# Performance work log

Measured on AMD Instinct MI355X. Metric: run time of the kernel, lower is better.

## Reference

```python
import jax, jax.numpy as jnp
import numpy as np

N_HEADS = 16
NEG = -1e9  # matches torch masked_fill value


def setup_inputs() -> dict:
    key = jax.random.key(0)
    ks = jax.random.split(key, 8)
    B, S, E = 4, 1024, 1024
    x = jax.random.normal(ks[0], (B, S, E), dtype=jnp.float32)
    event_lengths = jax.random.randint(ks[1], (B,), 1, S + 1)
    scale = 1.0 / np.sqrt(E)
    Wq = jax.random.normal(ks[2], (E, E), dtype=jnp.float32) * scale
    bq = jnp.zeros((E,), dtype=jnp.float32)
    Wk = jax.random.normal(ks[3], (E, E), dtype=jnp.float32) * scale
    bk = jnp.zeros((E,), dtype=jnp.float32)
    Wv = jax.random.normal(ks[4], (E, E), dtype=jnp.float32) * scale
    bv = jnp.zeros((E,), dtype=jnp.float32)
    return {"x": x, "Wq": Wq, "bq": bq, "Wk": Wk, "bk": bk,
            "Wv": Wv, "bv": bv, "event_lengths": event_lengths}


def reference(x, Wq, bq, Wk, bk, Wv, bv, event_lengths):
    B, S, E = x.shape
    H = N_HEADS
    D = E // H
    # fused projections, then split heads: [B,S,E] -> [B,H,S,D]
    def split(t):
        return t.reshape(B, S, H, D).transpose(0, 2, 1, 3)
    q = split(x @ Wq + bq)
    k = split(x @ Wk + bk)
    v = split(x @ Wv + bv)
    scores = jnp.einsum('bhsd,bhtd->bhst', q, k) / jnp.sqrt(jnp.float32(D))
    # rectangular length mask: valid iff row < len AND col < len
    idx = jnp.arange(S)
    valid = idx[None, :] < event_lengths[:, None]           # [B,S]
    mask = valid[:, :, None] & valid[:, None, :]            # [B,S,S]
    scores = jnp.where(mask[:, None, :, :], scores, NEG)
    attn = jax.nn.softmax(scores, axis=-1)
    out = jnp.einsum('bhst,bhtd->bhsd', attn, v)            # [B,H,S,D]
    # concat heads (== torch.cat over head outputs); NOTE: summarize proj is
    # dead code in the original (its result is overwritten), dropout is eval-identity
    return out.transpose(0, 2, 1, 3).reshape(B, S, E)
```

## Files before the change

kernel.cpp:

```cpp
#include <hip/hip_runtime.h>
#include <stdint.h>


using u16     = unsigned short;
using half8   = __attribute__((ext_vector_type(8))) _Float16;
using floatx4 = __attribute__((ext_vector_type(4))) float;

#define MFMA16(a, b, c) __builtin_amdgcn_mfma_f32_16x16x32_f16(a, b, c, 0, 0, 0)

__device__ __forceinline__ u16 f2h(float f) {
  _Float16 h = (_Float16)f; u16 u; __builtin_memcpy(&u, &h, 2); return u;
}

__device__ __forceinline__ void async_cp16(void* lds, const void* g) {
  __builtin_amdgcn_global_load_lds(
      (__attribute__((address_space(1))) uint32_t*)(uintptr_t)g,
      (__attribute__((address_space(3))) uint32_t*)(uint32_t)(uintptr_t)lds,
      16, 0, 0);
}

__global__ void k_prep(const float* __restrict__ x, u16* __restrict__ xh,
                       const float* __restrict__ w0, const float* __restrict__ w1,
                       const float* __restrict__ w2,
                       u16* __restrict__ o0, u16* __restrict__ o1,
                       u16* __restrict__ o2, float* __restrict__ vsum) {
  __shared__ float t[32][33];
  const int bx = blockIdx.x;
  if (bx < 4096) {
    int i = (bx * 256 + threadIdx.x) * 4;
    float4 v = *(const float4*)(x + i);
    ushort4 hv;
    hv.x = f2h(v.x);
    hv.y = f2h(v.y);
    hv.z = f2h(v.z);
    hv.w = f2h(v.w);
    *(ushort4*)(xh + i) = hv;
    if (bx == 0) {
      float4 z = {0.f, 0.f, 0.f, 0.f};
#pragma unroll
      for (int e = 0; e < 4; e++) ((float4*)vsum)[threadIdx.x * 4 + e] = z;
    }
    return;
  }
  const int id = bx - 4096;
  const int z = id >> 10, rem = id & 1023;
  const float* W = z == 0 ? w0 : (z == 1 ? w1 : w2);
  u16* oh = z == 0 ? o0 : (z == 1 ? o1 : o2);
  const int kb = (rem & 31) * 32, nb = (rem >> 5) * 32;
  const int tx = threadIdx.x & 31, ty = threadIdx.x >> 5;
  for (int r = ty; r < 32; r += 8) t[r][tx] = W[(kb + r) * 1024 + nb + tx];
  __syncthreads();
  for (int r = ty; r < 32; r += 8)
    oh[(nb + r) * 1024 + kb + tx] = f2h(t[tx][r]);
}

__launch_bounds__(256, 4)
__global__ void k_proj(const u16* __restrict__ xh,
                       const u16* __restrict__ wqT, const u16* __restrict__ wkT,
                       const u16* __restrict__ wvT,
                       const float* __restrict__ bq, const float* __restrict__ bk,
                       const float* __restrict__ bv,
                       const int* __restrict__ elen,
                       u16* __restrict__ qh, u16* __restrict__ kh,
                       u16* __restrict__ vth, float* __restrict__ vsum) {
  __shared__ u16 Sm[17408];
  const int z = blockIdx.z;
  const int m0 = blockIdx.x * 128, n0 = blockIdx.y * 128;
  if (z != 2 && (m0 & 1023) >= elen[m0 >> 10]) return;

  const u16* wT = z == 0 ? wqT : (z == 1 ? wkT : wvT);
  const float* bias = z == 0 ? bq : (z == 1 ? bk : bv);
  u16* oh = z == 0 ? qh : (z == 1 ? kh : vth);
  const float oscale = (z == 0) ? 0.18033688011112042f : 1.0f;

  const int tid = threadIdx.x, l = tid & 63, w = tid >> 6;
  const int quad = l >> 4, col = l & 15;
  const int wm = (w & 1) * 64, wn = (w >> 1) * 64;

  const int row0 = tid >> 3, ch = tid & 7;
  const int sc8 = (ch ^ (row0 & 7)) * 8;
  int gofs[4], lofs[4];
#pragma unroll
  for (int p = 0; p < 4; p++) {
    gofs[p] = (row0 + 32 * p) * 1024 + sc8;
    lofs[p] = (tid + p * 256) * 8;
  }

  const u16* Ag = xh + m0 * 1024;
  const u16* Bg = wT + n0 * 1024;

  int ar[2][4], br[2][4];
#pragma unroll
  for (int ks = 0; ks < 2; ks++) {
#pragma unroll
    for (int i = 0; i < 4; i++) {
      int r = wm + i * 16 + col;
      ar[ks][i] = r * 64 + (((ks * 4 + quad) ^ (r & 7)) * 8);
    }
#pragma unroll
    for (int j = 0; j < 4; j++) {
      int r = wn + j * 16 + col;
      br[ks][j] = r * 64 + (((ks * 4 + quad) ^ (r & 7)) * 8);
    }
  }

  floatx4 zero4 = {0.f, 0.f, 0.f, 0.f};
  floatx4 acc[4][4];
#pragma unroll
  for (int i = 0; i < 4; i++)
#pragma unroll
    for (int j = 0; j < 4; j++) acc[i][j] = zero4;

  for (int k0 = 0; k0 < 1024; k0 += 64) {
    __syncthreads();
#pragma unroll
    for (int p = 0; p < 4; p++) async_cp16(Sm + lofs[p], Ag + gofs[p] + k0);
#pragma unroll
    for (int p = 0; p < 4; p++)
      async_cp16(Sm + 8192 + lofs[p], Bg + gofs[p] + k0);
    __syncthreads();

#pragma unroll
    for (int ks = 0; ks < 2; ks++) {
      half8 fa[4], fb[4];
#pragma unroll
      for (int i = 0; i < 4; i++) fa[i] = *(const half8*)(Sm + ar[ks][i]);
#pragma unroll
      for (int j = 0; j < 4; j++)
        fb[j] = *(const half8*)(Sm + 8192 + br[ks][j]);
#pragma unroll
      for (int i = 0; i < 4; i++)
#pragma unroll
        for (int j = 0; j < 4; j++) acc[i][j] = MFMA16(fa[i], fb[j], acc[i][j]);
    }
  }

  const int bidx = m0 >> 10;
  const int sbase = m0 & 1023;
  __syncthreads();

#pragma unroll
  for (int j = 0; j < 4; j++) {
    int nloc = wn + j * 16 + col;
    float bb = bias[n0 + nloc];
#pragma unroll
    for (int i = 0; i < 4; i++)
#pragma unroll
      for (int r = 0; r < 4; r++) {
        int mloc = wm + i * 16 + quad * 4 + r;
        Sm[mloc * 136 + nloc] = f2h((acc[i][j][r] + bb) * oscale);
      }
  }
  __syncthreads();

  if (z != 2) {
#pragma unroll
    for (int k = 0; k < 8; k++) {
      int c = tid + k * 256;
      int mloc = c >> 4, n = (c & 15) * 8;
      int hh = (n0 + n) >> 6, d = (n0 + n) & 63;
      half8 vv = *(const half8*)(Sm + mloc * 136 + n);
      *(half8*)(oh + ((bidx * 16 + hh) * 1024 + sbase + mloc) * 64 + d) = vv;
    }
  } else {
#pragma unroll
    for (int k = 0; k < 8; k++) {
      int c = tid + k * 256;
      int nloc = c & 127, s0 = (c >> 7) * 8;
      int hh = (n0 + nloc) >> 6, d = (n0 + nloc) & 63;
      u16 tmp[8];
#pragma unroll
      for (int e = 0; e < 8; e++) tmp[e] = Sm[(s0 + e) * 136 + nloc];
      *(half8*)(vth + ((bidx * 16 + hh) * 64 + d) * 1024 + sbase + s0) =
          *(half8*)tmp;
    }
#pragma unroll
    for (int j = 0; j < 4; j++) {
      int nloc = wn + j * 16 + col;
      float bb = bias[n0 + nloc];
      float part = 16.0f * bb;
#pragma unroll
      for (int i = 0; i < 4; i++)
#pragma unroll
        for (int r = 0; r < 4; r++) part += acc[i][j][r];
      part += __shfl_xor(part, 16, 64);
      part += __shfl_xor(part, 32, 64);
      if (quad == 0) {
        int hh = (n0 + nloc) >> 6, d = (n0 + nloc) & 63;
        unsafeAtomicAdd(vsum + (bidx * 16 + hh) * 64 + d, part);
      }
    }
  }
}

__device__ __forceinline__ void stage64(u16* lds, const u16* g, int row_stride,
                                        int tid) {
#pragma unroll
  for (int p = 0; p < 2; p++) {
    int slot = (p * 256 + tid) * 8;
    int row = slot >> 6;
    int gp = (slot >> 3) & 7;
    int gl = gp ^ (row & 7);
    async_cp16(lds + slot, g + row * row_stride + gl * 8);
  }
}

__launch_bounds__(256)
__global__ void k_attn(const u16* __restrict__ qh_g,
                       const u16* __restrict__ kh_g,
                       const u16* __restrict__ vth_g,
                       const float* __restrict__ vsum, const int* __restrict__ elen,
                       float* __restrict__ out) {
  __shared__ u16 QP[4096];
  __shared__ u16 Bufs[2][8192];
  const int tid = threadIdx.x, l = tid & 63, w = tid >> 6;
  const int quad = l >> 4, col = l & 15;
  const int id = blockIdx.x;
  const int b = (id + (id >> 8)) & 3;
  const int h = (id >> 2) & 15;
  const int bh = b * 16 + h;
  const int q0 = ((id >> 6) & 15) * 64;
  const int len = elen[b];

  if (q0 >= len) {
    float val = vsum[bh * 64 + l] * (1.0f / 1024.0f);
    float* op = out + (b * 1024 + q0) * 1024 + h * 64 + l;
    for (int r = w; r < 64; r += 4) op[r * 1024] = val;
    return;
  }

  const u16* kh_b  = kh_g + bh * 65536;
  const u16* vth_b = vth_g + bh * 65536;

  stage64(QP, qh_g + (bh * 1024 + q0) * 64, 64, tid);
  stage64(Bufs[0], kh_b, 64, tid);
  stage64(Bufs[0] + 4096, vth_b, 1024, tid);
  __syncthreads();

  half8 qf[4][2];
#pragma unroll
  for (int jq = 0; jq < 4; jq++) {
    int qrow = jq * 16 + col;
#pragma unroll
    for (int ks = 0; ks < 2; ks++)
      qf[jq][ks] = *(const half8*)(QP + qrow * 64 +
                                   (((ks * 4 + quad) ^ (qrow & 7)) * 8));
  }

  int ko[2];
#pragma unroll
  for (int ks = 0; ks < 2; ks++) {
    int r = w * 16 + col;
    ko[ks] = r * 64 + (((ks * 4 + quad) ^ (r & 7)) * 8);
  }
  int kvo[2][4];
#pragma unroll
  for (int ks = 0; ks < 2; ks++)
#pragma unroll
    for (int j = 0; j < 4; j++) {
      int n = j * 16 + col;
      kvo[ks][j] = n * 64 + (((ks * 4 + quad) ^ (n & 7)) * 8);
    }
  int p_wr[4];
  {
    int chv = w * 2 + (quad >> 1);
#pragma unroll
    for (int jq = 0; jq < 4; jq++) {
      int row = jq * 16 + col;
      p_wr[jq] = row * 64 + ((chv ^ (row & 7)) * 8) + (quad & 1) * 4;
    }
  }

  floatx4 zero4 = {0.f, 0.f, 0.f, 0.f};
  floatx4 O[4];
  float lp[4];
#pragma unroll
  for (int j = 0; j < 4; j++) O[j] = zero4;
#pragma unroll
  for (int jq = 0; jq < 4; jq++) lp[jq] = 0.f;

  const int ntt = (len + 63) >> 6;
  for (int tt = 0; tt < ntt; ++tt) {
    const int t0 = tt * 64;
    u16* cur = Bufs[tt & 1];
    if (tt + 1 < ntt) {
      u16* nxt = Bufs[(tt + 1) & 1];
      const int t1 = t0 + 64;
      stage64(nxt, kh_b + t1 * 64, 64, tid);
      stage64(nxt + 4096, vth_b + t1, 1024, tid);
    }

    floatx4 sc[4];
#pragma unroll
    for (int jq = 0; jq < 4; jq++) sc[jq] = zero4;
#pragma unroll
    for (int ks = 0; ks < 2; ks++) {
      half8 kf = *(const half8*)(cur + ko[ks]);
#pragma unroll
      for (int jq = 0; jq < 4; jq++) sc[jq] = MFMA16(kf, qf[jq][ks], sc[jq]);
    }

    if (t0 + 64 > len) {
#pragma unroll
      for (int r = 0; r < 4; r++) {
        bool inv = (t0 + w * 16 + quad * 4 + r) >= len;
#pragma unroll
        for (int jq = 0; jq < 4; jq++)
          if (inv) sc[jq][r] = -3e38f;
      }
    }

#pragma unroll
    for (int jq = 0; jq < 4; jq++) {
      float e0 = __builtin_exp2f(sc[jq][0]);
      float e1 = __builtin_exp2f(sc[jq][1]);
      float e2 = __builtin_exp2f(sc[jq][2]);
      float e3 = __builtin_exp2f(sc[jq][3]);
      lp[jq] += (e0 + e1) + (e2 + e3);
      uint2 pk;
      pk.x = (uint32_t)f2h(e0) | ((uint32_t)f2h(e1) << 16);
      pk.y = (uint32_t)f2h(e2) | ((uint32_t)f2h(e3) << 16);
      *(uint2*)(QP + p_wr[jq]) = pk;
    }

    asm volatile("s_waitcnt lgkmcnt(0)" ::: "memory");
    __builtin_amdgcn_s_barrier();
    __builtin_amdgcn_sched_barrier(0);

#pragma unroll
    for (int ks = 0; ks < 2; ks++) {
      half8 pa = *(const half8*)(QP + ko[ks]);
#pragma unroll
      for (int j = 0; j < 4; j++) {
        half8 vb = *(const half8*)(cur + 4096 + kvo[ks][j]);
        O[j] = MFMA16(pa, vb, O[j]);
      }
    }

    __syncthreads();
  }

  float* lred = (float*)Bufs;
#pragma unroll
  for (int jq = 0; jq < 4; jq++) {
    float v = lp[jq];
    v += __shfl_xor(v, 16, 64);
    v += __shfl_xor(v, 32, 64);
    lp[jq] = v;
  }
  if (quad == 0) {
#pragma unroll
    for (int jq = 0; jq < 4; jq++) lred[w * 64 + jq * 16 + col] = lp[jq];
  }
  __syncthreads();

#pragma unroll
  for (int r = 0; r < 4; r++) {
    int qloc = w * 16 + quad * 4 + r;
    int s = q0 + qloc;
    float lr = (lred[qloc] + lred[64 + qloc]) +
               (lred[128 + qloc] + lred[192 + qloc]);
    float invl = 1.0f / lr;
    bool valid = (s < len);
#pragma unroll
    for (int j = 0; j < 4; j++) {
      int d = j * 16 + col;
      float val = valid ? O[j][r] * invl : vsum[bh * 64 + d] * (1.0f / 1024.0f);
      out[(b * 1024 + s) * 1024 + h * 64 + d] = val;
    }
  }
}

extern "C" void kernel_launch(void* const* d_in, const int* in_sizes, int n_in,
                              void* d_out, int out_size, void* d_ws, size_t ws_size,
                              hipStream_t stream) {
  (void)in_sizes; (void)n_in; (void)out_size; (void)ws_size;
  const float* x  = (const float*)d_in[0];
  const float* Wq = (const float*)d_in[1];
  const float* bq = (const float*)d_in[2];
  const float* Wk = (const float*)d_in[3];
  const float* bk = (const float*)d_in[4];
  const float* Wv = (const float*)d_in[5];
  const float* bv = (const float*)d_in[6];
  const int* elen = (const int*)d_in[7];
  float* out = (float*)d_out;

  char* ws = (char*)d_ws;
  const size_t MB = 1024 * 1024;
  u16* xh  = (u16*)(ws + 0 * MB);
  u16* wqT = (u16*)(ws + 8 * MB);
  u16* wkT = (u16*)(ws + 10 * MB);
  u16* wvT = (u16*)(ws + 12 * MB);
  u16* qh  = (u16*)(ws + 14 * MB);
  u16* kh  = (u16*)(ws + 22 * MB);
  u16* vth = (u16*)(ws + 30 * MB);
  float* vsum = (float*)(ws + 38 * MB);

  k_prep<<<7168, 256, 0, stream>>>(x, xh, Wq, Wk, Wv, wqT, wkT, wvT, vsum);
  k_proj<<<dim3(32, 8, 3), 256, 0, stream>>>(xh, wqT, wkT, wvT, bq, bk, bv,
                                             elen, qh, kh, vth, vsum);
  k_attn<<<1024, 256, 0, stream>>>(qh, kh, vth, vsum, elen, out);
}
```

Baseline: 149.2 us.

## Double attention query tile to 128 rows with 512-thread blocks sharing K/V stages

```diff
diff --git a/kernel.cpp b/kernel.cpp
--- a/kernel.cpp
+++ b/kernel.cpp
@@ -193,11 +193,12 @@
   }
 }
 
-__device__ __forceinline__ void stage64(u16* lds, const u16* g, int row_stride,
-                                        int tid) {
-#pragma unroll
-  for (int p = 0; p < 2; p++) {
-    int slot = (p * 256 + tid) * 8;
+template <int NC>
+__device__ __forceinline__ void stageN(u16* lds, const u16* g, int row_stride,
+                                       int tid) {
+#pragma unroll
+  for (int p = 0; p < NC; p++) {
+    int slot = (p * 512 + tid) * 8;
     int row = slot >> 6;
     int gp = (slot >> 3) & 7;
     int gl = gp ^ (row & 7);
@@ -205,53 +206,62 @@
   }
 }
 
-__launch_bounds__(256)
+__launch_bounds__(512)
 __global__ void k_attn(const u16* __restrict__ qh_g,
                        const u16* __restrict__ kh_g,
                        const u16* __restrict__ vth_g,
                        const float* __restrict__ vsum, const int* __restrict__ elen,
                        float* __restrict__ out) {
-  __shared__ u16 QP[4096];
+  __shared__ u16 QP[8192];
   __shared__ u16 Bufs[2][8192];
   const int tid = threadIdx.x, l = tid & 63, w = tid >> 6;
   const int quad = l >> 4, col = l & 15;
+  const int tb = w & 3;
+  const int qh2 = w >> 2;
   const int id = blockIdx.x;
   const int b = (id + (id >> 8)) & 3;
   const int h = (id >> 2) & 15;
   const int bh = b * 16 + h;
-  const int q0 = ((id >> 6) & 15) * 64;
+  const int q0 = ((id >> 6) & 7) * 128;
   const int len = elen[b];
 
   if (q0 >= len) {
     float val = vsum[bh * 64 + l] * (1.0f / 1024.0f);
     float* op = out + (b * 1024 + q0) * 1024 + h * 64 + l;
-    for (int r = w; r < 64; r += 4) op[r * 1024] = val;
+    for (int r = w; r < 128; r += 8) op[r * 1024] = val;
     return;
   }
 
   const u16* kh_b  = kh_g + bh * 65536;
   const u16* vth_b = vth_g + bh * 65536;
 
-  stage64(QP, qh_g + (bh * 1024 + q0) * 64, 64, tid);
-  stage64(Bufs[0], kh_b, 64, tid);
-  stage64(Bufs[0] + 4096, vth_b, 1024, tid);
+  stageN<2>(QP, qh_g + (bh * 1024 + q0) * 64, 64, tid);
+  stageN<1>(Bufs[0], kh_b, 64, tid);
+  stageN<1>(Bufs[0] + 4096, vth_b, 1024, tid);
   __syncthreads();
 
   half8 qf[4][2];
 #pragma unroll
-  for (int jq = 0; jq < 4; jq++) {
-    int qrow = jq * 16 + col;
+  for (int jj = 0; jj < 4; jj++) {
+    int qrow = (qh2 * 4 + jj) * 16 + col;
 #pragma unroll
     for (int ks = 0; ks < 2; ks++)
-      qf[jq][ks] = *(const half8*)(QP + qrow * 64 +
+      qf[jj][ks] = *(const half8*)(QP + qrow * 64 +
                                    (((ks * 4 + quad) ^ (qrow & 7)) * 8));
   }
+  __syncthreads();
 
   int ko[2];
+#pragma unroll
+  for (int ks = 0; ks < 2; ks++) {
+    int r = tb * 16 + col;
+    ko[ks] = r * 64 + (((ks * 4 + quad) ^ (r & 7)) * 8);
+  }
+  int po[2];
 #pragma unroll
   for (int ks = 0; ks < 2; ks++) {
     int r = w * 16 + col;
-    ko[ks] = r * 64 + (((ks * 4 + quad) ^ (r & 7)) * 8);
+    po[ks] = r * 64 + (((ks * 4 + quad) ^ (r & 7)) * 8);
   }
   int kvo[2][4];
 #pragma unroll
@@ -263,11 +273,11 @@
     }
   int p_wr[4];
   {
-    int chv = w * 2 + (quad >> 1);
-#pragma unroll
-    for (int jq = 0; jq < 4; jq++) {
-      int row = jq * 16 + col;
-      p_wr[jq] = row * 64 + ((chv ^ (row & 7)) * 8) + (quad & 1) * 4;
+    int chv = tb * 2 + (quad >> 1);
+#pragma unroll
+    for (int jj = 0; jj < 4; jj++) {
+      int row = (qh2 * 4 + jj) * 16 + col;
+      p_wr[jj] = row * 64 + ((chv ^ (row & 7)) * 8) + (quad & 1) * 4;
     }
   }
 
@@ -277,7 +287,7 @@
 #pragma unroll
   for (int j = 0; j < 4; j++) O[j] = zero4;
 #pragma unroll
-  for (int jq = 0; jq < 4; jq++) lp[jq] = 0.f;
+  for (int jj = 0; jj < 4; jj++) lp[jj] = 0.f;
 
   const int ntt = (len + 63) >> 6;
   for (int tt = 0; tt < ntt; ++tt) {
@@ -286,41 +296,41 @@
     if (tt + 1 < ntt) {
       u16* nxt = Bufs[(tt + 1) & 1];
       const int t1 = t0 + 64;
-      stage64(nxt, kh_b + t1 * 64, 64, tid);
-      stage64(nxt + 4096, vth_b + t1, 1024, tid);
+      stageN<1>(nxt, kh_b + t1 * 64, 64, tid);
+      stageN<1>(nxt + 4096, vth_b + t1, 1024, tid);
     }
 
     floatx4 sc[4];
 #pragma unroll
-    for (int jq = 0; jq < 4; jq++) sc[jq] = zero4;
+    for (int jj = 0; jj < 4; jj++) sc[jj] = zero4;
 #pragma unroll
     for (int ks = 0; ks < 2; ks++) {
       half8 kf = *(const half8*)(cur + ko[ks]);
 #pragma unroll
-      for (int jq = 0; jq < 4; jq++) sc[jq] = MFMA16(kf, qf[jq][ks], sc[jq]);
+      for (int jj = 0; jj < 4; jj++) sc[jj] = MFMA16(kf, qf[jj][ks], sc[jj]);
     }
 
     if (t0 + 64 > len) {
 #pragma unroll
       for (int r = 0; r < 4; r++) {
-        bool inv = (t0 + w * 16 + quad * 4 + r) >= len;
-#pragma unroll
-        for (int jq = 0; jq < 4; jq++)
-          if (inv) sc[jq][r] = -3e38f;
+        bool inv = (t0 + tb * 16 + quad * 4 + r) >= len;
+#pragma unroll
+        for (int jj = 0; jj < 4; jj++)
+          if (inv) sc[jj][r] = -3e38f;
       }
     }
 
 #pragma unroll
-    for (int jq = 0; jq < 4; jq++) {
-      float e0 = __builtin_exp2f(sc[jq][0]);
-      float e1 = __builtin_exp2f(sc[jq][1]);
-      float e2 = __builtin_exp2f(sc[jq][2]);
-      float e3 = __builtin_exp2f(sc[jq][3]);
-      lp[jq] += (e0 + e1) + (e2 + e3);
+    for (int jj = 0; jj < 4; jj++) {
+      float e0 = __builtin_exp2f(sc[jj][0]);
+      float e1 = __builtin_exp2f(sc[jj][1]);
+      float e2 = __builtin_exp2f(sc[jj][2]);
+      float e3 = __builtin_exp2f(sc[jj][3]);
+      lp[jj] += (e0 + e1) + (e2 + e3);
       uint2 pk;
       pk.x = (uint32_t)f2h(e0) | ((uint32_t)f2h(e1) << 16);
       pk.y = (uint32_t)f2h(e2) | ((uint32_t)f2h(e3) << 16);
-      *(uint2*)(QP + p_wr[jq]) = pk;
+      *(uint2*)(QP + p_wr[jj]) = pk;
     }
 
     asm volatile("s_waitcnt lgkmcnt(0)" ::: "memory");
@@ -329,7 +339,7 @@
 
 #pragma unroll
     for (int ks = 0; ks < 2; ks++) {
-      half8 pa = *(const half8*)(QP + ko[ks]);
+      half8 pa = *(const half8*)(QP + po[ks]);
 #pragma unroll
       for (int j = 0; j < 4; j++) {
         half8 vb = *(const half8*)(cur + 4096 + kvo[ks][j]);
@@ -342,15 +352,16 @@
 
   float* lred = (float*)Bufs;
 #pragma unroll
-  for (int jq = 0; jq < 4; jq++) {
-    float v = lp[jq];
+  for (int jj = 0; jj < 4; jj++) {
+    float v = lp[jj];
     v += __shfl_xor(v, 16, 64);
     v += __shfl_xor(v, 32, 64);
-    lp[jq] = v;
+    lp[jj] = v;
   }
   if (quad == 0) {
 #pragma unroll
-    for (int jq = 0; jq < 4; jq++) lred[w * 64 + jq * 16 + col] = lp[jq];
+    for (int jj = 0; jj < 4; jj++)
+      lred[tb * 128 + (qh2 * 4 + jj) * 16 + col] = lp[jj];
   }
   __syncthreads();
 
@@ -358,8 +369,8 @@
   for (int r = 0; r < 4; r++) {
     int qloc = w * 16 + quad * 4 + r;
     int s = q0 + qloc;
-    float lr = (lred[qloc] + lred[64 + qloc]) +
-               (lred[128 + qloc] + lred[192 + qloc]);
+    float lr = (lred[qloc] + lred[128 + qloc]) +
+               (lred[256 + qloc] + lred[384 + qloc]);
     float invl = 1.0f / lr;
     bool valid = (s < len);
 #pragma unroll
@@ -399,5 +410,5 @@
   k_prep<<<7168, 256, 0, stream>>>(x, xh, Wq, Wk, Wv, wqT, wkT, wvT, vsum);
   k_proj<<<dim3(32, 8, 3), 256, 0, stream>>>(xh, wqT, wkT, wvT, bq, bk, bv,
                                              elen, qh, kh, vth, vsum);
-  k_attn<<<1024, 256, 0, stream>>>(qh, kh, vth, vsum, elen, out);
-}
+  k_attn<<<512, 512, 0, stream>>>(qh, kh, vth, vsum, elen, out);
+}
```

After: 148.7 us, median of 3. Within noise of the previous version (-0.3%).
